# Optimization experiments

Measured on AMD Instinct MI355X. Metric: run time of the kernel, lower is better.

## Reference

```python
import jax, jax.numpy as jnp
import numpy as np

B, D = 8192, 1024
C, K = 1000, 8
EPS = 1e-15


def setup_inputs() -> dict:
    key = jax.random.key(0)
    k1, k2 = jax.random.split(key)
    # points inside the unit Poincare ball (c=1): scale so E||x|| ~ 0.64 < 1
    x = jax.random.normal(k1, (B, D), dtype=jnp.float32) * 0.02
    weight_v = jax.random.normal(k2, (C, K, D), dtype=jnp.float32)
    weight_g = jnp.ones((C,), dtype=jnp.float32)
    gamma = jnp.ones((), dtype=jnp.float32)
    return {"x": x, "weight_v": weight_v, "weight_g": weight_g, "gamma": gamma}


def reference(x, weight_v, weight_g, gamma):
    # PoincareBall curvature c = 1.0 -> rc = sqrt(c) = 1.0
    rc = jnp.asarray(1.0, dtype=x.dtype)
    # unit prototype directions: [C, K, D]
    z_norm = jnp.maximum(jnp.linalg.norm(weight_v, axis=-1, keepdims=True), EPS)
    z_unit = weight_v / z_norm
    rcx = rc * x                                   # [B, D]
    cx2 = jnp.sum(rcx * rcx, axis=-1, keepdims=True)  # [B, 1]
    inner = jnp.einsum('bd,ckd->bck', rcx, z_unit)    # [B, C, K]
    drcr = 2.0 * rc * gamma
    num = 2.0 * inner * jnp.cosh(drcr) - (1.0 + cx2[:, :, None]) * jnp.sinh(drcr)
    den = jnp.maximum(1.0 - cx2, EPS)              # [B, 1]
    logits_ck = (2.0 * weight_g[None, :, None] / rc) * jnp.arcsinh(num / den[:, :, None])
    logits = jax.nn.logsumexp(logits_ck, axis=-1)  # [B, C]
    return logits
```

## Files before the change

### kernel.cpp

```cpp
#include <hip/hip_runtime.h>
#include <hip/hip_bf16.h>
#include <stdint.h>

#define B_ROWS 8192
#define D_DIM  1024
#define C_CLS  1000
#define K_PROT 8
#define N_PAD  8064
#define BM2    256
#define BN2    128
#define BKT    64
#define NTI    16

typedef __attribute__((ext_vector_type(8))) short  short8;
typedef __attribute__((ext_vector_type(4))) float  f32x4;


__device__ __forceinline__ ushort f2bf(float f) {
    union { float f; uint32_t u; } v; v.f = f;
    uint32_t u = v.u;
    return (ushort)((u + 0x7fffu + ((u >> 16) & 1u)) >> 16);
}

typedef __attribute__((address_space(1))) void gv_t;
typedef __attribute__((address_space(3))) void lv_t;

__device__ __forceinline__ void gload_lds16(const void* g, void* l) {
    __builtin_amdgcn_global_load_lds((gv_t*)g, (lv_t*)l, 16, 0, 0);
}

__device__ __forceinline__ float waveReduceSum(float s) {
    #pragma unroll
    for (int m = 32; m >= 1; m >>= 1) s += __shfl_xor(s, m);
    return s;
}


__global__ __launch_bounds__(256) void prep_z(const float* __restrict__ wv,
                                              ushort* __restrict__ zb) {
    const int P = blockIdx.x;
    const int t = threadIdx.x;
    __shared__ float red[4];

    const int gpan = P >> 6;
    const int ni   = (P >> 4) & 3;
    const int cc   = P & 15;
    const int cls  = gpan * 8 + (cc & 7);
    const int k    = ni + ((cc >> 3) << 2);

    if (cls >= C_CLS) {
        ((ushort4*)(zb + (size_t)P * D_DIM))[t] = make_ushort4(0, 0, 0, 0);
        return;
    }
    const int n = cls * K_PROT + k;
    const float4 v = ((const float4*)(wv + (size_t)n * D_DIM))[t];
    float s = v.x*v.x + v.y*v.y + v.z*v.z + v.w*v.w;
    s = waveReduceSum(s);
    if ((t & 63) == 0) red[t >> 6] = s;
    __syncthreads();
    const float n2 = red[0] + red[1] + red[2] + red[3];
    const float rn = 1.0f / fmaxf(sqrtf(n2), 1e-15f);
    ushort4 o;
    o.x = f2bf(v.x * rn); o.y = f2bf(v.y * rn);
    o.z = f2bf(v.z * rn); o.w = f2bf(v.w * rn);
    ((ushort4*)(zb + (size_t)P * D_DIM))[t] = o;
}


__global__ __launch_bounds__(256) void prep_x(const float* __restrict__ x,
                                              ushort* __restrict__ xb,
                                              float* __restrict__ cx2) {
    const int b = blockIdx.x;
    const int t = threadIdx.x;
    __shared__ float red[4];

    const float4 v = ((const float4*)(x + (size_t)b * D_DIM))[t];
    ushort4 o;
    o.x = f2bf(v.x); o.y = f2bf(v.y); o.z = f2bf(v.z); o.w = f2bf(v.w);
    ((ushort4*)(xb + (size_t)b * D_DIM))[t] = o;

    float s = v.x*v.x + v.y*v.y + v.z*v.z + v.w*v.w;
    s = waveReduceSum(s);
    if ((t & 63) == 0) red[t >> 6] = s;
    __syncthreads();
    if (t == 0) cx2[b] = red[0] + red[1] + red[2] + red[3];
}


__global__ __launch_bounds__(256, 2) void gemm_epi(
        const ushort* __restrict__ A,
        const ushort* __restrict__ Bz,
        const float*  __restrict__ cx2g,
        const float*  __restrict__ wgl,
        const float*  __restrict__ gamma_p,
        float*        __restrict__ out)
{
    __shared__ __attribute__((aligned(16))) ushort sA[BM2 * BKT];
    __shared__ __attribute__((aligned(16))) ushort sB[BN2 * BKT];

    const int tid  = threadIdx.x;
    const int lane = tid & 63;
    const int w    = tid >> 6;
    const int wm   = w >> 1;
    const int wn   = w & 1;

    const int bm = blockIdx.x & 31;
    const int bn = blockIdx.x >> 5;
    const int m0 = bm * BM2;
    const int n0 = bn * BN2;

    const int stCol = ((lane & 7) ^ (lane >> 3)) * 8;
    const ushort* aS = A  + (size_t)(m0 + (tid >> 3)) * D_DIM + stCol;
    const ushort* bS = Bz + (size_t)(n0 + (tid >> 3)) * D_DIM + stCol;

    const int swz0 = ((      (lane >> 4) * 16) ^ ((lane & 7) << 4));
    const int swz1 = ((64 + ((lane >> 4) * 16)) ^ ((lane & 7) << 4));
    const char* sAb = (const char*)sA + (wm * 128 + (lane & 15)) * 128;
    const char* sBb = (const char*)sB + (wn * 64  + (lane & 15)) * 128;

    f32x4 acc[8][4];
    #pragma unroll
    for (int mi = 0; mi < 8; ++mi)
        #pragma unroll
        for (int ni = 0; ni < 4; ++ni)
            acc[mi][ni] = (f32x4)(0.0f);

    for (int t = 0; t < NTI; ++t) {
        const int k0 = t * BKT;
        #pragma unroll
        for (int i = 0; i < 8; ++i)
            gload_lds16(aS + (size_t)i * 32 * D_DIM + k0,
                        (char*)sA + i * 4096 + w * 1024);
        #pragma unroll
        for (int i = 0; i < 4; ++i)
            gload_lds16(bS + (size_t)i * 32 * D_DIM + k0,
                        (char*)sB + i * 4096 + w * 1024);
        __syncthreads();

        #pragma unroll
        for (int kk = 0; kk < 2; ++kk) {
            const int swzk = kk ? swz1 : swz0;
            short8 a[8], b[4];
            #pragma unroll
            for (int mi = 0; mi < 8; ++mi)
                a[mi] = *(const short8*)(sAb + mi * 16 * 128 + swzk);
            #pragma unroll
            for (int ni = 0; ni < 4; ++ni)
                b[ni] = *(const short8*)(sBb + ni * 16 * 128 + swzk);
            #pragma unroll
            for (int mi = 0; mi < 8; ++mi)
                #pragma unroll
                for (int ni = 0; ni < 4; ++ni)
                    acc[mi][ni] = __builtin_amdgcn_mfma_f32_16x16x32_bf16(
                        a[mi], b[ni], acc[mi][ni], 0, 0, 0);
        }
        __syncthreads();
    }

    float* scx = (float*)sA;
    scx[tid] = cx2g[m0 + tid];
    __syncthreads();

    const float gam = gamma_p[0];
    const float ex  = expf(2.0f * gam);
    const float ch2 = ex + 1.0f / ex;
    const float sh  = 0.5f * (ex - 1.0f / ex);

    const int  pan = (n0 >> 6) + wn;
    const int  cls = pan * 8 + (lane & 7);
    const bool wrt = ((lane & 8) == 0) && (cls < C_CLS);
    const float w2 = (cls < C_CLS) ? 2.0f * wgl[cls] : 0.0f;

    #pragma unroll
    for (int mi = 0; mi < 8; ++mi) {
        #pragma unroll
        for (int r = 0; r < 4; ++r) {
            const int mloc = wm * 128 + mi * 16 + ((lane >> 4) << 2) + r;
            const float c2   = scx[mloc];
            const float rden = 1.0f / fmaxf(1.0f - c2, 1e-15f);
            const float tc   = ch2 * rden;
            const float tp   = (1.0f + c2) * sh * rden;
            float bk[4];
            #pragma unroll
            for (int ni = 0; ni < 4; ++ni) {
                const float t = fmaf(acc[mi][ni][r], tc, -tp);
                const float u = fmaxf(t + __fsqrt_rn(fmaf(t, t, 1.0f)), 1e-20f);
                bk[ni] = w2 * __logf(u);
            }
            float mx = fmaxf(fmaxf(bk[0], bk[1]), fmaxf(bk[2], bk[3]));
            mx = fmaxf(mx, __shfl_xor(mx, 8));
            float s = __expf(bk[0] - mx) + __expf(bk[1] - mx)
                    + __expf(bk[2] - mx) + __expf(bk[3] - mx);
            s += __shfl_xor(s, 8);
            if (wrt)
                out[(size_t)(m0 + mloc) * C_CLS + cls] = mx + __logf(s);
        }
    }
}


extern "C" void kernel_launch(void* const* d_in, const int* in_sizes, int n_in,
                              void* d_out, int out_size, void* d_ws, size_t ws_size,
                              hipStream_t stream) {
    const float* x     = (const float*)d_in[0];
    const float* wv    = (const float*)d_in[1];
    const float* wg    = (const float*)d_in[2];
    const float* gamma = (const float*)d_in[3];
    float* out = (float*)d_out;

    char* ws = (char*)d_ws;
    ushort* xb  = (ushort*)ws;
    ushort* zb  = (ushort*)(ws + (size_t)B_ROWS * D_DIM * 2);
    float*  cx2 = (float*)(ws + (size_t)B_ROWS * D_DIM * 2
                              + (size_t)N_PAD * D_DIM * 2);

    prep_z<<<N_PAD, 256, 0, stream>>>(wv, zb);
    prep_x<<<B_ROWS, 256, 0, stream>>>(x, xb, cx2);
    gemm_epi<<<32 * 63, 256, 0, stream>>>(xb, zb, cx2, wg, gamma, out);
}
```

Baseline: 170.7 us.

## Enlarge GEMM tile to 256x256 with 8 waves, XCD-aware block mapping, merge prep kernels

Doubles the N tile of the bf16 MFMA GEMM to 256 and uses 512-thread blocks (8 waves in a 2x4 grid), giving each block more operand reuse per LDS load. Block indices are remapped so that the blocks on each XCD share the same N panels, aiming at better L2 locality. The two prep kernels are merged into one launch to cut launch overhead. N is padded to 8192, which adds wasted work on padding rows, and the larger LDS footprint and 512-thread blocks may reduce occupancy.

```diff
diff --git a/kernel.cpp b/kernel.cpp
--- a/kernel.cpp
+++ b/kernel.cpp
@@ -6,11 +6,11 @@
 #define D_DIM  1024
 #define C_CLS  1000
 #define K_PROT 8
-#define N_PAD  8064
-#define BM2    256
-#define BN2    128
+#define N_PAD  8192
+#define BM     256
+#define BN     256
 #define BKT    64
-#define NTI    16
+#define NT     16
 
 typedef __attribute__((ext_vector_type(8))) short  short8;
 typedef __attribute__((ext_vector_type(4))) float  f32x4;
@@ -36,12 +36,29 @@
 }
 
 
-__global__ __launch_bounds__(256) void prep_z(const float* __restrict__ wv,
-                                              ushort* __restrict__ zb) {
-    const int P = blockIdx.x;
+__global__ __launch_bounds__(256) void prep(const float* __restrict__ x,
+                                            const float* __restrict__ wv,
+                                            ushort* __restrict__ xb,
+                                            ushort* __restrict__ zb,
+                                            float* __restrict__ cx2) {
     const int t = threadIdx.x;
     __shared__ float red[4];
 
+    if ((int)blockIdx.x < B_ROWS) {
+        const int b = blockIdx.x;
+        const float4 v = ((const float4*)(x + (size_t)b * D_DIM))[t];
+        ushort4 o;
+        o.x = f2bf(v.x); o.y = f2bf(v.y); o.z = f2bf(v.z); o.w = f2bf(v.w);
+        ((ushort4*)(xb + (size_t)b * D_DIM))[t] = o;
+        float s = v.x*v.x + v.y*v.y + v.z*v.z + v.w*v.w;
+        s = waveReduceSum(s);
+        if ((t & 63) == 0) red[t >> 6] = s;
+        __syncthreads();
+        if (t == 0) cx2[b] = red[0] + red[1] + red[2] + red[3];
+        return;
+    }
+
+    const int P    = blockIdx.x - B_ROWS;
     const int gpan = P >> 6;
     const int ni   = (P >> 4) & 3;
     const int cc   = P & 15;
@@ -67,27 +84,7 @@
 }
 
 
-__global__ __launch_bounds__(256) void prep_x(const float* __restrict__ x,
-                                              ushort* __restrict__ xb,
-                                              float* __restrict__ cx2) {
-    const int b = blockIdx.x;
-    const int t = threadIdx.x;
-    __shared__ float red[4];
-
-    const float4 v = ((const float4*)(x + (size_t)b * D_DIM))[t];
-    ushort4 o;
-    o.x = f2bf(v.x); o.y = f2bf(v.y); o.z = f2bf(v.z); o.w = f2bf(v.w);
-    ((ushort4*)(xb + (size_t)b * D_DIM))[t] = o;
-
-    float s = v.x*v.x + v.y*v.y + v.z*v.z + v.w*v.w;
-    s = waveReduceSum(s);
-    if ((t & 63) == 0) red[t >> 6] = s;
-    __syncthreads();
-    if (t == 0) cx2[b] = red[0] + red[1] + red[2] + red[3];
-}
-
-
-__global__ __launch_bounds__(256, 2) void gemm_epi(
+__global__ __launch_bounds__(512, 2) void gemm_epi(
         const ushort* __restrict__ A,
         const ushort* __restrict__ Bz,
         const float*  __restrict__ cx2g,
@@ -95,23 +92,27 @@
         const float*  __restrict__ gamma_p,
         float*        __restrict__ out)
 {
-    __shared__ __attribute__((aligned(16))) ushort sA[BM2 * BKT];
-    __shared__ __attribute__((aligned(16))) ushort sB[BN2 * BKT];
+    __shared__ __attribute__((aligned(16))) ushort sA[BM * BKT];
+    __shared__ __attribute__((aligned(16))) ushort sB[BN * BKT];
 
     const int tid  = threadIdx.x;
     const int lane = tid & 63;
-    const int w    = tid >> 6;
-    const int wm   = w >> 1;
-    const int wn   = w & 1;
-
-    const int bm = blockIdx.x & 31;
-    const int bn = blockIdx.x >> 5;
-    const int m0 = bm * BM2;
-    const int n0 = bn * BN2;
-
-    const int stCol = ((lane & 7) ^ (lane >> 3)) * 8;
+    const int wid  = tid >> 6;
+    const int wm   = wid >> 2;
+    const int wn   = wid & 3;
+
+    const int bid = blockIdx.x;
+    const int xcd = bid & 7;
+    const int j   = bid >> 3;
+    const int bn  = xcd * 4 + (j & 3);
+    const int bm  = j >> 2;
+    const int m0  = bm * BM;
+    const int n0  = bn * BN;
+
+    const int stCol = ((tid & 7) ^ ((tid >> 3) & 7)) * 8;
     const ushort* aS = A  + (size_t)(m0 + (tid >> 3)) * D_DIM + stCol;
     const ushort* bS = Bz + (size_t)(n0 + (tid >> 3)) * D_DIM + stCol;
+    const int ldsW = wid * 1024;
 
     const int swz0 = ((      (lane >> 4) * 16) ^ ((lane & 7) << 4));
     const int swz1 = ((64 + ((lane >> 4) * 16)) ^ ((lane & 7) << 4));
@@ -125,16 +126,16 @@
         for (int ni = 0; ni < 4; ++ni)
             acc[mi][ni] = (f32x4)(0.0f);
 
-    for (int t = 0; t < NTI; ++t) {
+    for (int t = 0; t < NT; ++t) {
         const int k0 = t * BKT;
         #pragma unroll
-        for (int i = 0; i < 8; ++i)
-            gload_lds16(aS + (size_t)i * 32 * D_DIM + k0,
-                        (char*)sA + i * 4096 + w * 1024);
-        #pragma unroll
         for (int i = 0; i < 4; ++i)
-            gload_lds16(bS + (size_t)i * 32 * D_DIM + k0,
-                        (char*)sB + i * 4096 + w * 1024);
+            gload_lds16(aS + (size_t)i * 64 * D_DIM + k0,
+                        (char*)sA + i * 8192 + ldsW);
+        #pragma unroll
+        for (int i = 0; i < 4; ++i)
+            gload_lds16(bS + (size_t)i * 64 * D_DIM + k0,
+                        (char*)sB + i * 8192 + ldsW);
         __syncthreads();
 
         #pragma unroll
@@ -158,7 +159,7 @@
     }
 
     float* scx = (float*)sA;
-    scx[tid] = cx2g[m0 + tid];
+    if (tid < 256) scx[tid] = cx2g[m0 + tid];
     __syncthreads();
 
     const float gam = gamma_p[0];
@@ -214,7 +215,6 @@
     float*  cx2 = (float*)(ws + (size_t)B_ROWS * D_DIM * 2
                               + (size_t)N_PAD * D_DIM * 2);
 
-    prep_z<<<N_PAD, 256, 0, stream>>>(wv, zb);
-    prep_x<<<B_ROWS, 256, 0, stream>>>(x, xb, cx2);
-    gemm_epi<<<32 * 63, 256, 0, stream>>>(xb, zb, cx2, wg, gamma, out);
-}
+    prep<<<B_ROWS + N_PAD, 256, 0, stream>>>(x, wv, xb, zb, cx2);
+    gemm_epi<<<1024, 512, 0, stream>>>(xb, zb, cx2, wg, gamma, out);
+}
```

Measured after the change: 205.7 us. +20.5%, slower.
